# Performance work log

Hardware: AMD Instinct MI355X
Metric: run time of the kernel (lower is better)

## Reference

```python
import jax, jax.numpy as jnp
import numpy as np

# --- hashgrid config (from __init__: num_levels=16, level_dim=4, base_res=2, log2_hashmap_size=19, desired_res=2048) ---
NUM_LEVELS = 16
LEVEL_DIM = 4
BASE_RES = 2
DESIRED_RES = 2048
TABLE_SIZE = 2 ** 19
_b = np.exp((np.log(DESIRED_RES) - np.log(BASE_RES)) / (NUM_LEVELS - 1))
SCALES = BASE_RES * _b ** np.arange(NUM_LEVELS) - 1.0          # instant-ngp per-level scale
RES = (np.ceil(SCALES) + 1).astype(np.int64)                   # per-level grid resolution
PRIME = np.uint32(2654435761)                                  # 2D spatial hash prime


def softplus10(x):
    return jax.nn.softplus(10.0 * x) / 10.0


def hash_encode(u, tables):
    """u: [P,2] in [0,1]; tables: [L, TABLE_SIZE, LEVEL_DIM]. Returns [P, L*LEVEL_DIM]."""
    outs = []
    for l in range(NUM_LEVELS):
        s = float(SCALES[l])
        res = int(RES[l])
        pos = u * s + 0.5
        pf = jnp.floor(pos)
        fr = pos - pf                      # bilinear fractions, [P,2]
        pi = pf.astype(jnp.int32)
        acc = None
        for dx in (0, 1):
            for dy in (0, 1):
                cx = pi[:, 0] + dx
                cy = pi[:, 1] + dy
                if res * res <= TABLE_SIZE:
                    idx = cy * res + cx                                   # dense level
                else:
                    idx = (cx.astype(jnp.uint32) ^ (cy.astype(jnp.uint32) * PRIME)) % jnp.uint32(TABLE_SIZE)
                    idx = idx.astype(jnp.int32)                           # hashed level
                wx = fr[:, 0] if dx else 1.0 - fr[:, 0]
                wy = fr[:, 1] if dy else 1.0 - fr[:, 1]
                term = tables[l][idx] * (wx * wy)[:, None]                # gather + bilerp
                acc = term if acc is None else acc + term
        outs.append(acc)
    return jnp.concatenate(outs, axis=-1)


def setup_inputs() -> dict:
    key = jax.random.key(0)
    ks = jax.random.split(key, 4)
    B, N, T = 4, 2048, 192
    x = jax.random.normal(ks[0], (B, N, T, 2), jnp.float32)
    embeddings = jax.random.normal(ks[1], (NUM_LEVELS, TABLE_SIZE, LEVEL_DIM), jnp.float32) * 1e-2
    W0 = jax.random.normal(ks[2], (64, 64), jnp.float32) / 8.0
    b0 = jnp.zeros((64,), jnp.float32)
    W1 = jax.random.normal(ks[3], (64, 1), jnp.float32) / 8.0
    b1 = jnp.zeros((1,), jnp.float32)
    return {"x": x, "embeddings": embeddings, "W0": W0, "b0": b0, "W1": W1, "b1": b1}


def reference(x, embeddings, W0, b0, W1, b1):
    B, N, T = x.shape[:3]
    xf = x.reshape(-1, T, 2)                       # [B*N, T, 2]
    rays_o = xf[:, 0]
    rd = xf[:, -1] - xf[:, 0]
    rd = rd / jnp.linalg.norm(rd, axis=-1, keepdims=True)
    z = jnp.linspace(0.0, 2.0, T)                  # [T]
    sample_dist = 1.0 / T
    xys = rays_o[:, None, :] + rd[:, None, :] * z[None, :, None]   # [B*N, T, 2]
    xys = jnp.clip(xys, -1.0, 1.0)                 # aabb clamp [-1,-1,1,1]
    u = (xys.reshape(-1, 2) + 1.0) * 0.5           # map [-bound,bound] -> [0,1], bound=1
    feats = hash_encode(u, embeddings)             # [P, 64]
    h = softplus10(feats @ W0 + b0)
    sigma = softplus10(h @ W1 + b1).reshape(-1, T) # [B*N, T]
    deltas = jnp.concatenate([jnp.full((1,), sample_dist, sigma.dtype), z[1:] - z[:-1]])  # [T]
    density = (deltas[None, :] * sigma).reshape(B, N, T)
    return density
```

## Files before the change

### kernel.cpp

```cpp
#include <hip/hip_runtime.h>
#include <cmath>
#include <algorithm>

#define NUM_LEVELS 16
#define TABLE_SIZE 524288
#define TMASK (TABLE_SIZE - 1)
#define HASH_PRIME 2654435761u
#define T_SAMPLES 192
#define BLOCK 256
#define PTS 64
#define CHUNK 4096
#define N_RAYS 8192

typedef _Float16 f16;
typedef f16 f16x4 __attribute__((ext_vector_type(4)));
typedef f16 f16x8 __attribute__((ext_vector_type(8)));
typedef float f32x4 __attribute__((ext_vector_type(4)));

struct LvlParams {
    float s[NUM_LEVELS];
    int   res[NUM_LEVELS];
    int   mode[NUM_LEVELS];
    int   offB[NUM_LEVELS];
    int   used[NUM_LEVELS];
};

#define C_10L2E  14.42695040888963f
#define C_LN2_01 0.0693147180559945f

#define EXP2F(x) __builtin_amdgcn_exp2f(x)
#define LOG2F(x) __builtin_amdgcn_logf(x)

__device__ __forceinline__ float softplus10(float x) {
    float t = 10.0f * x;
    float e = __expf(-fabsf(t));
    return (fmaxf(t, 0.0f) + __logf(1.0f + e)) * 0.1f;
}

__device__ __forceinline__ f16x4 lerp4h(f16x4 c00, f16x4 c01, f16x4 c10, f16x4 c11,
                                        float fx, float fy) {
    float gx = 1.0f - fx, gy = 1.0f - fy;
    f16 w00 = (f16)(gx * gy), w01 = (f16)(gx * fy);
    f16 w10 = (f16)(fx * gy), w11 = (f16)(fx * fy);
    f16x4 v00 = {w00, w00, w00, w00}, v01 = {w01, w01, w01, w01};
    f16x4 v10 = {w10, w10, w10, w10}, v11 = {w11, w11, w11, w11};
    return c00 * v00 + c01 * v01 + c10 * v10 + c11 * v11;
}

__device__ __forceinline__ f16x4 lerp4f(f32x4 c00, f32x4 c01, f32x4 c10, f32x4 c11,
                                        float fx, float fy) {
    float w00 = (1.0f - fx) * (1.0f - fy), w01 = (1.0f - fx) * fy;
    float w10 = fx * (1.0f - fy),          w11 = fx * fy;
    f32x4 a = c00 * w00 + c01 * w01 + c10 * w10 + c11 * w11;
    return __builtin_convertvector(a, f16x4);
}

__global__ void prep_tables(const float* __restrict__ emb, char* __restrict__ embq,
                            const float* __restrict__ W0, f16* __restrict__ w0f,
                            const float* __restrict__ x, float* __restrict__ rayBuf,
                            const LvlParams lp) {
    const int t = threadIdx.x;
    if (blockIdx.x == 0 && blockIdx.y == 0) {
        #pragma unroll
        for (int i = 0; i < 16; ++i) {
            int f = t * 16 + i;
            int j = f & 7, lx = (f >> 3) & 15, q = (f >> 7) & 3, nt = (f >> 9) & 3, kc = f >> 11;
            w0f[f] = (f16)W0[(kc * 32 + q * 8 + j) * 64 + (nt * 16 + lx)];
        }
    }
    if (blockIdx.y == 1 && blockIdx.x < (N_RAYS / 256)) {
        const int ray = blockIdx.x * 256 + t;
        const float2 o  = *(const float2*)(x + (size_t)ray * (T_SAMPLES * 2));
        const float2 ep = *(const float2*)(x + (size_t)ray * (T_SAMPLES * 2) + (T_SAMPLES - 1) * 2);
        float rdx = ep.x - o.x, rdy = ep.y - o.y;
        float inv = 1.0f / sqrtf(rdx * rdx + rdy * rdy);
        f32x4 rb; rb.x = o.x; rb.y = o.y; rb.z = rdx * inv; rb.w = rdy * inv;
        *(f32x4*)(rayBuf + (size_t)ray * 4) = rb;
    }
    const int l    = blockIdx.y;
    const int used = lp.used[l];
    const int base = blockIdx.x * CHUNK;
    if (base >= used) return;
    const float* src = emb + (size_t)l * TABLE_SIZE * 4;
    char* dst = embq + lp.offB[l];
    if (lp.mode[l] == 1) {
        const int res = lp.res[l];
        #pragma unroll
        for (int i = 0; i < 16; ++i) {
            int e = base + t + 256 * i;
            if (e < used) {
                f32x4 v00 = *(const f32x4*)(src + (size_t)e * 4);
                f32x4 v10 = *(const f32x4*)(src + (size_t)(e + 1) * 4);
                f32x4 v01 = *(const f32x4*)(src + (size_t)(e + res) * 4);
                f32x4 v11 = *(const f32x4*)(src + (size_t)(e + res + 1) * 4);
                f16x4 a = __builtin_convertvector(v00, f16x4);
                f16x4 b = __builtin_convertvector(v10, f16x4);
                f16x4 c = __builtin_convertvector(v01, f16x4);
                f16x4 d = __builtin_convertvector(v11, f16x4);
                f16x8 q0 = __builtin_shufflevector(a, b, 0, 1, 2, 3, 4, 5, 6, 7);
                f16x8 q1 = __builtin_shufflevector(c, d, 0, 1, 2, 3, 4, 5, 6, 7);
                *(f16x8*)(dst + ((size_t)e << 5))      = q0;
                *(f16x8*)(dst + ((size_t)e << 5) + 16) = q1;
            }
        }
    } else {
        #pragma unroll
        for (int i = 0; i < 16; ++i) {
            int e = base + t + 256 * i;
            if (e < used) {
                f32x4 v = *(const f32x4*)(src + (size_t)e * 4);
                *(f16x4*)(dst + (size_t)e * 8) = __builtin_convertvector(v, f16x4);
            }
        }
    }
}

template<bool QT>
__launch_bounds__(BLOCK, 8)
__global__ void nerf_fused(const float* __restrict__ x,
                           const float* __restrict__ emb,
                           const char* __restrict__ embq,
                           const f16* __restrict__ w0f,
                           const float* __restrict__ rayBuf,
                           const float* __restrict__ b0,
                           const float* __restrict__ W1,
                           const float* __restrict__ b1,
                           float* __restrict__ out,
                           const LvlParams lp) {
    __shared__ __align__(16) f16 feT[NUM_LEVELS * PTS * 4];

    const int tid  = threadIdx.x;
    const int lane = tid & 63;
    const int w    = __builtin_amdgcn_readfirstlane(tid >> 6);

    const int ray = blockIdx.x / 3;
    const int t   = (blockIdx.x - ray * 3) * PTS + lane;
    const float z = (float)((double)t * (2.0 / 191.0));

    float ux, uy;
    if (QT) {
        const f32x4 rb = *(const f32x4*)(rayBuf + (size_t)ray * 4);
        float px = fminf(fmaxf(rb.x + rb.z * z, -1.0f), 1.0f);
        float py = fminf(fmaxf(rb.y + rb.w * z, -1.0f), 1.0f);
        ux = (px + 1.0f) * 0.5f;
        uy = (py + 1.0f) * 0.5f;
    } else {
        const float2 o  = *(const float2*)(x + (size_t)ray * (T_SAMPLES * 2));
        const float2 ep = *(const float2*)(x + (size_t)ray * (T_SAMPLES * 2) + (T_SAMPLES - 1) * 2);
        float rdx = ep.x - o.x, rdy = ep.y - o.y;
        float inv = 1.0f / sqrtf(rdx * rdx + rdy * rdy);
        rdx *= inv; rdy *= inv;
        float px = fminf(fmaxf(o.x + rdx * z, -1.0f), 1.0f);
        float py = fminf(fmaxf(o.y + rdy * z, -1.0f), 1.0f);
        ux = (px + 1.0f) * 0.5f;
        uy = (py + 1.0f) * 0.5f;
    }

    if (QT) {
        f16x4 c00[4], c01[4], c10[4], c11[4];
        float fxs[4], fys[4];
        #pragma unroll
        for (int li = 0; li < 4; ++li) {
            const int l = w + li * 4;
            const int mode = lp.mode[l];
            const float s = lp.s[l];
            float posx = ux * s + 0.5f, posy = uy * s + 0.5f;
            float pfx = floorf(posx), pfy = floorf(posy);
            fxs[li] = posx - pfx; fys[li] = posy - pfy;
            int cx = (int)pfx, cy = (int)pfy;
            const char* lb = embq + lp.offB[l];
            if (mode == 2) {
                unsigned hy0 = (unsigned)cy * HASH_PRIME;
                unsigned hy1 = hy0 + HASH_PRIME;
                int iA  = (int)(((unsigned)cx ^ hy0) & TMASK);
                int iB  = (int)(((unsigned)cx ^ hy1) & TMASK);
                int iA1 = (int)(((unsigned)(cx + 1) ^ hy0) & TMASK);
                int iB1 = (int)(((unsigned)(cx + 1) ^ hy1) & TMASK);
                c00[li] = *(const f16x4*)(lb + ((size_t)iA  << 3));
                c01[li] = *(const f16x4*)(lb + ((size_t)iB  << 3));
                c10[li] = *(const f16x4*)(lb + ((size_t)iA1 << 3));
                c11[li] = *(const f16x4*)(lb + ((size_t)iB1 << 3));
            } else if (mode == 1) {
                int i00 = cy * lp.res[l] + cx;
                f16x8 q0 = *(const f16x8*)(lb + ((size_t)i00 << 5));
                f16x8 q1 = *(const f16x8*)(lb + ((size_t)i00 << 5) + 16);
                c00[li] = __builtin_shufflevector(q0, q0, 0, 1, 2, 3);
                c10[li] = __builtin_shufflevector(q0, q0, 4, 5, 6, 7);
                c01[li] = __builtin_shufflevector(q1, q1, 0, 1, 2, 3);
                c11[li] = __builtin_shufflevector(q1, q1, 4, 5, 6, 7);
            } else {
                const int res = lp.res[l];
                int i00 = cy * res + cx;
                const f16x4* tb = (const f16x4*)lb;
                c00[li] = tb[i00];       c10[li] = tb[i00 + 1];
                c01[li] = tb[i00 + res]; c11[li] = tb[i00 + res + 1];
            }
        }
        #pragma unroll
        for (int li = 0; li < 4; ++li) {
            const int l = w + li * 4;
            *(f16x4*)&feT[(l * PTS + lane) * 4] =
                lerp4h(c00[li], c01[li], c10[li], c11[li], fxs[li], fys[li]);
        }
    } else {
        #pragma unroll
        for (int li = 0; li < 4; ++li) {
            const int l = w + li * 4;
            const float s = lp.s[l];
            float posx = ux * s + 0.5f, posy = uy * s + 0.5f;
            float pfx = floorf(posx), pfy = floorf(posy);
            float fx = posx - pfx, fy = posy - pfy;
            int cx = (int)pfx, cy = (int)pfy;
            int i00, i01, i10, i11;
            if (lp.mode[l] == 2) {
                unsigned hy0 = (unsigned)cy * HASH_PRIME;
                unsigned hy1 = hy0 + HASH_PRIME;
                i00 = (int)(((unsigned)cx ^ hy0) & TMASK);
                i01 = (int)(((unsigned)cx ^ hy1) & TMASK);
                i10 = (int)(((unsigned)(cx + 1) ^ hy0) & TMASK);
                i11 = (int)(((unsigned)(cx + 1) ^ hy1) & TMASK);
            } else {
                const int res = lp.res[l];
                i00 = cy * res + cx; i10 = i00 + 1;
                i01 = i00 + res;     i11 = i01 + 1;
            }
            const f32x4* tb = (const f32x4*)(emb + (size_t)l * (TABLE_SIZE * 4));
            f32x4 a = tb[i00], b = tb[i01], c = tb[i10], d = tb[i11];
            *(f16x4*)&feT[(l * PTS + lane) * 4] = lerp4f(a, b, c, d, fx, fy);
        }
    }

    const int lx = lane & 15, q = lane >> 4;
    float b0l2[4], w1l2[4];
    #pragma unroll
    for (int nt = 0; nt < 4; ++nt) {
        b0l2[nt] = b0[nt * 16 + lx] * C_10L2E;
        w1l2[nt] = W1[nt * 16 + lx] * C_LN2_01;
    }
    const float b1v = b1[0];

    __syncthreads();

    const int p = w * 16 + lx;

    f32x4 acc[4];
    #pragma unroll
    for (int nt = 0; nt < 4; ++nt) acc[nt] = (f32x4)(0.0f);

    #pragma unroll
    for (int kc = 0; kc < 2; ++kc) {
        const int la = kc * 8 + 2 * q;
        f16x4 lo = *(const f16x4*)&feT[(la * PTS + p) * 4];
        f16x4 hi = *(const f16x4*)&feT[((la + 1) * PTS + p) * 4];
        f16x8 afr = __builtin_shufflevector(lo, hi, 0, 1, 2, 3, 4, 5, 6, 7);
        #pragma unroll
        for (int nt = 0; nt < 4; ++nt) {
            f16x8 bfr = *(const f16x8*)(w0f + (size_t)(((kc * 4 + nt) * 4 + q) * 16 + lx) * 8);
            acc[nt] = __builtin_amdgcn_mfma_f32_16x16x32_f16(afr, bfr, acc[nt], 0, 0, 0);
        }
    }

    const float d0 = (float)(1.0 / 192.0);
    const float d1 = (float)(2.0 / 191.0);

    float part[4];
    #pragma unroll
    for (int r = 0; r < 4; ++r) {
        float pp = 0.0f;
        #pragma unroll
        for (int nt = 0; nt < 4; ++nt) {
            float t2 = fmaf(acc[nt][r], C_10L2E, b0l2[nt]);
            float e2 = EXP2F(-fabsf(t2));
            float sp = fmaxf(t2, 0.0f) + LOG2F(1.0f + e2);
            pp = fmaf(sp, w1l2[nt], pp);
        }
        pp += __shfl_xor(pp, 1, 64);
        pp += __shfl_xor(pp, 2, 64);
        pp += __shfl_xor(pp, 4, 64);
        pp += __shfl_xor(pp, 8, 64);
        part[r] = pp;
    }
    if (lx == 0) {
        const int g0 = blockIdx.x * PTS + w * 16 + q * 4;
        const int tt = g0 % T_SAMPLES;
        const float dd0 = d0 * C_LN2_01, dd1 = d1 * C_LN2_01;
        f32x4 ov;
        #pragma unroll
        for (int r = 0; r < 4; ++r) {
            float t2 = (part[r] + b1v) * C_10L2E;
            float e2 = EXP2F(-fabsf(t2));
            float sp = fmaxf(t2, 0.0f) + LOG2F(1.0f + e2);
            ov[r] = sp * ((r == 0 && tt == 0) ? dd0 : dd1);
        }
        *(f32x4*)(out + g0) = ov;
    }
}

extern "C" void kernel_launch(void* const* d_in, const int* in_sizes, int n_in,
                              void* d_out, int out_size, void* d_ws, size_t ws_size,
                              hipStream_t stream) {
    const float* x   = (const float*)d_in[0];
    const float* emb = (const float*)d_in[1];
    const float* W0  = (const float*)d_in[2];
    const float* b0  = (const float*)d_in[3];
    const float* W1  = (const float*)d_in[4];
    const float* b1  = (const float*)d_in[5];
    float* out = (float*)d_out;

    char*  ws     = (char*)d_ws;
    f16*   w0f    = (f16*)ws;
    float* rayBuf = (float*)(ws + 8192);
    char*  embq   = ws + 147456;

    LvlParams lp;
    const double bb = std::exp((std::log(2048.0) - std::log(2.0)) / 15.0);
    int offB = 0, maxUsed = 0;
    for (int l = 0; l < NUM_LEVELS; ++l) {
        double sc = 2.0 * std::pow(bb, (double)l) - 1.0;
        int rr = (int)std::ceil(sc) + 1;
        lp.s[l] = (float)sc;
        lp.res[l] = rr;
        const bool hashed = ((long long)rr * (long long)rr > (long long)TABLE_SIZE);
        int used;
        if (hashed) {
            used = TABLE_SIZE;
        } else {
            long long cmax = (long long)std::floor(sc + 0.5) + 1;
            long long u = cmax * (long long)rr + cmax + 1 + (rr + 2);
            used = (int)std::min((long long)TABLE_SIZE, u);
        }
        lp.mode[l] = hashed ? 2 : (rr >= 150 ? 1 : 0);
        lp.offB[l] = offB;
        lp.used[l] = used;
        const long long bytes = (lp.mode[l] == 1) ? (long long)used * 32
                                                  : (long long)used * 8;
        offB += (int)((bytes + 4095) & ~4095LL);
        if (used > maxUsed) maxUsed = used;
    }
    const size_t need = 147456 + (size_t)offB;
    const bool useQ = ws_size >= need;

    const int nblk = out_size / PTS;
    if (useQ) {
        dim3 pg((maxUsed + CHUNK - 1) / CHUNK, NUM_LEVELS);
        prep_tables<<<pg, 256, 0, stream>>>(emb, embq, W0, w0f, x, rayBuf, lp);
        nerf_fused<true><<<nblk, BLOCK, 0, stream>>>(x, emb, embq, w0f, rayBuf,
                                                     b0, W1, b1, out, lp);
    } else {
        dim3 pg1(1, 1);
        prep_tables<<<pg1, 256, 0, stream>>>(emb, embq, W0, w0f, x, rayBuf, lp);
        nerf_fused<false><<<nblk, BLOCK, 0, stream>>>(x, emb, embq, w0f, rayBuf,
                                                      b0, W1, b1, out, lp);
    }
}
```

Baseline: 335.1 us.

## Balance per-wave level assignment, pack feature pairs, stage W0 in LDS

Levels are now assigned to waves through a constant table that mixes cheap dense levels with costly hashed levels, so each wave does a similar amount of gather work. Features are stored in LDS as interleaved level pairs, so the MFMA A-fragment comes from one 16-byte LDS read instead of two 8-byte reads plus a shuffle. The W0 fragments are loaded cooperatively into LDS early in the kernel, replacing per-wave global reads inside the MFMA loop. This uses an extra 8 KB of shared memory per block, which may lower occupancy, and the level lookup becomes a constant-memory load.

```diff
diff --git a/kernel.cpp b/kernel.cpp
--- a/kernel.cpp
+++ b/kernel.cpp
@@ -31,11 +31,12 @@
 #define EXP2F(x) __builtin_amdgcn_exp2f(x)
 #define LOG2F(x) __builtin_amdgcn_logf(x)
 
-__device__ __forceinline__ float softplus10(float x) {
-    float t = 10.0f * x;
-    float e = __expf(-fabsf(t));
-    return (fmaxf(t, 0.0f) + __logf(1.0f + e)) * 0.1f;
-}
+__device__ __constant__ const int LVL[4][4] = {
+    {0, 1, 8, 13},
+    {2, 3, 7, 14},
+    {4, 5, 6, 15},
+    {9, 10, 11, 12},
+};
 
 __device__ __forceinline__ f16x4 lerp4h(f16x4 c00, f16x4 c01, f16x4 c10, f16x4 c11,
                                         float fx, float fy) {
@@ -127,11 +128,18 @@
                            const float* __restrict__ b1,
                            float* __restrict__ out,
                            const LvlParams lp) {
-    __shared__ __align__(16) f16 feT[NUM_LEVELS * PTS * 4];
+    __shared__ __align__(16) f16 feT2[8 * PTS * 8];
+    __shared__ __align__(16) f16 w0lds[4096];
 
     const int tid  = threadIdx.x;
     const int lane = tid & 63;
     const int w    = __builtin_amdgcn_readfirstlane(tid >> 6);
+
+    f16x8 wreg0, wreg1;
+    {
+        const f16x8* wp = (const f16x8*)(w0f + (size_t)tid * 16);
+        wreg0 = wp[0]; wreg1 = wp[1];
+    }
 
     const int ray = blockIdx.x / 3;
     const int t   = (blockIdx.x - ray * 3) * PTS + lane;
@@ -161,7 +169,7 @@
         float fxs[4], fys[4];
         #pragma unroll
         for (int li = 0; li < 4; ++li) {
-            const int l = w + li * 4;
+            const int l = LVL[w][li];
             const int mode = lp.mode[l];
             const float s = lp.s[l];
             float posx = ux * s + 0.5f, posy = uy * s + 0.5f;
@@ -196,16 +204,24 @@
                 c01[li] = tb[i00 + res]; c11[li] = tb[i00 + res + 1];
             }
         }
+        {
+            f16x8* wl = (f16x8*)&w0lds[(size_t)tid * 16];
+            wl[0] = wreg0; wl[1] = wreg1;
+        }
         #pragma unroll
         for (int li = 0; li < 4; ++li) {
-            const int l = w + li * 4;
-            *(f16x4*)&feT[(l * PTS + lane) * 4] =
-                lerp4h(c00[li], c01[li], c10[li], c11[li], fxs[li], fys[li]);
+            const int l = LVL[w][li];
+            f16x4 r = lerp4h(c00[li], c01[li], c10[li], c11[li], fxs[li], fys[li]);
+            *(f16x4*)&feT2[(((l >> 1) * PTS + lane) * 8) + (l & 1) * 4] = r;
         }
     } else {
+        {
+            f16x8* wl = (f16x8*)&w0lds[(size_t)tid * 16];
+            wl[0] = wreg0; wl[1] = wreg1;
+        }
         #pragma unroll
         for (int li = 0; li < 4; ++li) {
-            const int l = w + li * 4;
+            const int l = LVL[w][li];
             const float s = lp.s[l];
             float posx = ux * s + 0.5f, posy = uy * s + 0.5f;
             float pfx = floorf(posx), pfy = floorf(posy);
@@ -226,7 +242,8 @@
             }
             const f32x4* tb = (const f32x4*)(emb + (size_t)l * (TABLE_SIZE * 4));
             f32x4 a = tb[i00], b = tb[i01], c = tb[i10], d = tb[i11];
-            *(f16x4*)&feT[(l * PTS + lane) * 4] = lerp4f(a, b, c, d, fx, fy);
+            f16x4 r = lerp4f(a, b, c, d, fx, fy);
+            *(f16x4*)&feT2[(((l >> 1) * PTS + lane) * 8) + (l & 1) * 4] = r;
         }
     }
 
@@ -249,13 +266,10 @@
 
     #pragma unroll
     for (int kc = 0; kc < 2; ++kc) {
-        const int la = kc * 8 + 2 * q;
-        f16x4 lo = *(const f16x4*)&feT[(la * PTS + p) * 4];
-        f16x4 hi = *(const f16x4*)&feT[((la + 1) * PTS + p) * 4];
-        f16x8 afr = __builtin_shufflevector(lo, hi, 0, 1, 2, 3, 4, 5, 6, 7);
+        f16x8 afr = *(const f16x8*)&feT2[((kc * 4 + q) * PTS + p) * 8];
         #pragma unroll
         for (int nt = 0; nt < 4; ++nt) {
-            f16x8 bfr = *(const f16x8*)(w0f + (size_t)(((kc * 4 + nt) * 4 + q) * 16 + lx) * 8);
+            f16x8 bfr = *(const f16x8*)&w0lds[(size_t)(((kc * 4 + nt) * 4 + q) * 16 + lx) * 8];
             acc[nt] = __builtin_amdgcn_mfma_f32_16x16x32_f16(afr, bfr, acc[nt], 0, 0, 0);
         }
     }
```

New measurement: 324.9 us. 1.03x faster.
